# Optimization experiments

Measured on AMD Instinct MI355X. Metric: run time of the kernel, lower is better.

Reference implementation:

```python
import jax, jax.numpy as jnp
import numpy as np

BETA = 0.92
THRESHOLD = 1.0
SLOPE = 25.0  # snntorch surrogate.fast_sigmoid default slope


@jax.custom_vjp
def spike_fn(x):
    # Heaviside forward, fast-sigmoid surrogate backward
    return (x > 0).astype(x.dtype)


def _spike_fwd(x):
    return (x > 0).astype(x.dtype), x


def _spike_bwd(x, g):
    return (g / (SLOPE * jnp.abs(x) + 1.0) ** 2,)


spike_fn.defvjp(_spike_fwd, _spike_bwd)


def _lif(cur, mem_prev):
    # snntorch Leaky (reset_mechanism='subtract'): reset is based on the
    # PREVIOUS membrane and is detached from the graph.
    reset = jax.lax.stop_gradient((mem_prev > THRESHOLD).astype(cur.dtype))
    mem = BETA * mem_prev + cur - reset * THRESHOLD
    spk = spike_fn(mem - THRESHOLD)
    return spk, mem


def setup_inputs() -> dict:
    key = jax.random.key(0)
    ks = jax.random.split(key, 7)
    T, B, D_IN, H = 100, 4096, 9, 96
    return {
        "spike_input": (jax.random.uniform(ks[0], (T, B, D_IN)) < 0.3).astype(jnp.float32),
        "W1": jax.random.normal(ks[1], (H, D_IN), jnp.float32) * (1.0 / np.sqrt(D_IN)),
        "b1": jax.random.normal(ks[2], (H,), jnp.float32) * 0.01,
        "W2": jax.random.normal(ks[3], (H, H), jnp.float32) * (1.0 / np.sqrt(H)),
        "b2": jax.random.normal(ks[4], (H,), jnp.float32) * 0.01,
        "W3": jax.random.normal(ks[5], (H // 2, H), jnp.float32) * (1.0 / np.sqrt(H)),
        "b3": jax.random.normal(ks[6], (H // 2,), jnp.float32) * 0.01,
    }


def reference(spike_input, W1, b1, W2, b2, W3, b3):
    # spike_input: [T, B, input_dim]
    B = spike_input.shape[1]
    H = W1.shape[0]
    H3 = W3.shape[0]
    dt = spike_input.dtype
    init = (jnp.zeros((B, H), dt), jnp.zeros((B, H), dt), jnp.zeros((B, H3), dt))

    def step(carry, x_t):
        m1, m2, m3 = carry
        s1, m1 = _lif(x_t @ W1.T + b1, m1)
        s2, m2 = _lif(s1 @ W2.T + b2, m2)
        s3, m3 = _lif(s2 @ W3.T + b3, m3)
        return (m1, m2, m3), (s3, m3)

    _, (spk_rec, mem_rec) = jax.lax.scan(step, init, spike_input)
    # [T, B, hidden//2] each (fc_out is never applied in the original forward)
    return spk_rec, mem_rec
```

## Files before the change

kernel.cpp:

```cpp
#include <hip/hip_runtime.h>


constexpr int T_STEPS = 100;
constexpr int BATCH   = 4096;
constexpr int D_INP   = 9;
constexpr int H       = 96;
constexpr int H3      = 48;
constexpr int WAVES   = 8;
constexpr int BPW     = 2;
constexpr int NB      = WAVES * BPW;
constexpr int BLOCK   = WAVES * 64;
constexpr int NBLK    = BATCH / NB;

__device__ __forceinline__ float lif_step(float sum, float bias, float& m) {
    const float cur   = __fadd_rn(sum, bias);
    const float mp    = m;
    const float reset = (mp > 1.0f) ? 1.0f : 0.0f;
    const float mn    = __fsub_rn(__fadd_rn(__fmul_rn(0.92f, mp), cur), reset);
    m = mn;
    return mn;
}

#if defined(__has_builtin)
#if __has_builtin(__builtin_amdgcn_mov_dpp)
#define SNN_HAS_DPP 1
#endif
#endif

template <int CTRL>
__device__ __forceinline__ float xadd(float c) {
#ifdef SNN_HAS_DPP
    const int o = __builtin_amdgcn_mov_dpp(__float_as_int(c), CTRL, 0xF, 0xF, false);
    return __fadd_rn(c, __int_as_float(o));
#else
    return __fadd_rn(c, __shfl_xor(c, (CTRL == 0xB1) ? 1 : 2, 64));
#endif
}

__device__ __forceinline__ float quad_red(float c) {
    return xadd<0x4E>(xadd<0xB1>(c));
}

#define UNPACK2(dw, row)                                                      \
    sf[row][0]     = (float)( (dw)        & 255u);                            \
    sf[row][1]     = (float)(((dw) >> 8)  & 255u);                            \
    sf[(row)+1][0] = (float)(((dw) >> 16) & 255u);                            \
    sf[(row)+1][1] = (float)( (dw) >> 24);

#define FMA8(accv, wv, base)                                                  \
    accv[0] = fmaf(wv.x, sf[(base)+0][0], accv[0]);                           \
    accv[1] = fmaf(wv.x, sf[(base)+0][1], accv[1]);                           \
    accv[0] = fmaf(wv.y, sf[(base)+1][0], accv[0]);                           \
    accv[1] = fmaf(wv.y, sf[(base)+1][1], accv[1]);                           \
    accv[0] = fmaf(wv.z, sf[(base)+2][0], accv[0]);                           \
    accv[1] = fmaf(wv.z, sf[(base)+2][1], accv[1]);                           \
    accv[0] = fmaf(wv.w, sf[(base)+3][0], accv[0]);                           \
    accv[1] = fmaf(wv.w, sf[(base)+3][1], accv[1]);

__global__ __launch_bounds__(BLOCK, 2)
void snn_w8(const float* __restrict__ x,
            const float* __restrict__ W1g, const float* __restrict__ b1g,
            const float* __restrict__ W2g, const float* __restrict__ b2g,
            const float* __restrict__ W3g, const float* __restrict__ b3g,
            float* __restrict__ out)
{
    __shared__ __align__(16) float          W2L[36 * 64 * 4];
    __shared__ __align__(16) float          W3L[18 * 64 * 4];
    __shared__ __align__(16) float          W1L[96 * 12];
    __shared__ __align__(16) float          b1L[96], b2L[96], b3L[48];
    __shared__ __align__(16) unsigned short s1u[WAVES][4][24];
    __shared__ __align__(16) unsigned short s2u[WAVES][4][24];

    const int tid = threadIdx.x;
    const int w   = tid >> 6;
    const int l   = tid & 63;
    const int q   = l >> 2;
    const int r   = l & 3;
    const int r01 = r & 1;
    const int bL  = l >> 5;
    const int bg0 = blockIdx.x * NB + w * BPW;

    for (int idx = tid; idx < 36 * 64; idx += BLOCK) {
        const int c = idx >> 6, ll = idx & 63;
        const int s = c / 6, jq = c % 6, qq = ll >> 2, rr = ll & 3;
        #pragma unroll
        for (int jj = 0; jj < 4; ++jj)
            W2L[idx * 4 + jj] = W2g[(16 * s + qq) * H + 16 * jq + 4 * jj + rr];
    }
    for (int idx = tid; idx < 18 * 64; idx += BLOCK) {
        const int c = idx >> 6, ll = idx & 63;
        const int s = c / 6, jq = c % 6, qq = ll >> 2, rr = ll & 3;
        #pragma unroll
        for (int jj = 0; jj < 4; ++jj)
            W3L[idx * 4 + jj] = W3g[(16 * s + qq) * H + 16 * jq + 4 * jj + rr];
    }
    for (int idx = tid; idx < 96 * 12; idx += BLOCK) {
        const int n = idx / 12, k = idx % 12;
        W1L[idx] = (k < 9) ? W1g[n * D_INP + k] : 0.0f;
    }
    if (tid < 96) { b1L[tid] = b1g[tid]; b2L[tid] = b2g[tid]; }
    if (tid < 48) { b3L[tid] = b3g[tid]; }

    float m1[3] = {}, m2[6] = {}, m3[3] = {};

    const float* xp = x + (size_t)(bg0 + bL) * D_INP;
    float xr[D_INP];
    #pragma unroll
    for (int k = 0; k < D_INP; ++k) xr[k] = xp[k];

    float* ps = out + (size_t)(bg0 + r01) * H3 + q;
    float* pm = ps + (size_t)T_STEPS * BATCH * H3;

    __syncthreads();

    unsigned char* s1b = (unsigned char*)&s1u[w][0][0];
    unsigned char* s2b = (unsigned char*)&s2u[w][0][0];

    #pragma unroll 1
    for (int t = 0; t < T_STEPS; ++t) {
        #pragma unroll
        for (int i = 0; i < 3; ++i) {
            const int n1 = (l & 31) + 32 * i;
            const float4 wa = *(const float4*)&W1L[n1 * 12];
            const float4 wb = *(const float4*)&W1L[n1 * 12 + 4];
            const float  w8 = W1L[n1 * 12 + 8];
            const float q0 = __fmul_rn(wa.x, xr[0]);
            const float q1 = __fmul_rn(wa.y, xr[1]);
            const float q2 = __fmul_rn(wa.z, xr[2]);
            const float q3 = __fmul_rn(wa.w, xr[3]);
            const float q4 = __fmul_rn(wb.x, xr[4]);
            const float q5 = __fmul_rn(wb.y, xr[5]);
            const float q6 = __fmul_rn(wb.z, xr[6]);
            const float q7 = __fmul_rn(wb.w, xr[7]);
            const float q8 = __fmul_rn(w8,   xr[8]);
            const float r0 = __fadd_rn(__fadd_rn(q8, q0), q4);
            const float r1 = __fadd_rn(q1, q5);
            const float r2 = __fadd_rn(q2, q6);
            const float r3 = __fadd_rn(q3, q7);
            const float s  = __fadd_rn(__fadd_rn(r0, r1), __fadd_rn(r2, r3));
            const float mn = lif_step(s, b1L[n1], m1[i]);
            s1b[((n1 & 3) * 24 + (n1 >> 2)) * 2 + bL] =
                (mn > 1.0f) ? (unsigned char)1 : (unsigned char)0;
        }
        if (t + 1 < T_STEPS) {
            xp += (size_t)BATCH * D_INP;
            #pragma unroll
            for (int k = 0; k < D_INP; ++k) xr[k] = xp[k];
        }
        asm volatile("s_waitcnt lgkmcnt(0)" ::: "memory");

        {
            float acc[6][2] = {};
            #pragma unroll
            for (int jc = 0; jc < 3; ++jc) {
                const uint4 sp = *(const uint4*)&s1u[w][r][8 * jc];
                float sf[8][2];
                UNPACK2(sp.x, 0) UNPACK2(sp.y, 2) UNPACK2(sp.z, 4) UNPACK2(sp.w, 6)
                #pragma unroll
                for (int s = 0; s < 6; ++s) {
                    const float4 w0 = *(const float4*)&W2L[((s * 6 + 2 * jc)     * 64 + l) * 4];
                    const float4 w1 = *(const float4*)&W2L[((s * 6 + 2 * jc + 1) * 64 + l) * 4];
                    FMA8(acc[s], w0, 0)
                    FMA8(acc[s], w1, 4)
                }
            }
            #pragma unroll
            for (int s = 0; s < 6; ++s) {
                const float g0 = quad_red(acc[s][0]);
                const float g1 = quad_red(acc[s][1]);
                const float sv = r01 ? g1 : g0;
                const float mn = lif_step(sv, b2L[16 * s + q], m2[s]);
                if (r < 2) {
                    const int n2 = 16 * s + q;
                    s2b[((n2 & 3) * 24 + (n2 >> 2)) * 2 + r] =
                        (mn > 1.0f) ? (unsigned char)1 : (unsigned char)0;
                }
            }
        }
        asm volatile("s_waitcnt lgkmcnt(0)" ::: "memory");

        {
            float a3[3][2] = {};
            #pragma unroll
            for (int jc = 0; jc < 3; ++jc) {
                const uint4 sp = *(const uint4*)&s2u[w][r][8 * jc];
                float sf[8][2];
                UNPACK2(sp.x, 0) UNPACK2(sp.y, 2) UNPACK2(sp.z, 4) UNPACK2(sp.w, 6)
                #pragma unroll
                for (int s = 0; s < 3; ++s) {
                    const float4 w0 = *(const float4*)&W3L[((s * 6 + 2 * jc)     * 64 + l) * 4];
                    const float4 w1 = *(const float4*)&W3L[((s * 6 + 2 * jc + 1) * 64 + l) * 4];
                    FMA8(a3[s], w0, 0)
                    FMA8(a3[s], w1, 4)
                }
            }
            #pragma unroll
            for (int s = 0; s < 3; ++s) {
                const float g0 = quad_red(a3[s][0]);
                const float g1 = quad_red(a3[s][1]);
                const float sv = r01 ? g1 : g0;
                const float mn = lif_step(sv, b3L[16 * s + q], m3[s]);
                if (r < 2) {
                    ps[16 * s] = (mn > 1.0f) ? 1.0f : 0.0f;
                    pm[16 * s] = mn;
                }
            }
            ps += (size_t)BATCH * H3;
            pm += (size_t)BATCH * H3;
        }
    }
}

extern "C" void kernel_launch(void* const* d_in, const int* in_sizes, int n_in,
                              void* d_out, int out_size, void* d_ws, size_t ws_size,
                              hipStream_t stream)
{
    const float* x  = (const float*)d_in[0];
    const float* W1 = (const float*)d_in[1];
    const float* b1 = (const float*)d_in[2];
    const float* W2 = (const float*)d_in[3];
    const float* b2 = (const float*)d_in[4];
    const float* W3 = (const float*)d_in[5];
    const float* b3 = (const float*)d_in[6];
    float* out = (float*)d_out;

    snn_w8<<<dim3(NBLK), dim3(BLOCK), 0, stream>>>(
        x, W1, b1, W2, b2, W3, b3, out);
}
```

Baseline: 443.4 us.

## Batch four timesteps per iteration to reuse layer weights from LDS

The time loop is restructured into chunks of four steps. Layer-1 spikes for all four steps are computed first. The W2 and W3 LDS fragments are then loaded once per chunk and applied to all four spike vectors, and the LIF recurrences run sequentially afterwards. W1 and the biases move from shared memory into registers. The goal is to cut LDS weight traffic and the number of per-step waits, at the cost of much higher register pressure, with possible spills under the two-blocks-per-CU launch bound.

```diff
diff --git a/kernel.cpp b/kernel.cpp
--- a/kernel.cpp
+++ b/kernel.cpp
@@ -11,6 +11,7 @@
 constexpr int NB      = WAVES * BPW;
 constexpr int BLOCK   = WAVES * 64;
 constexpr int NBLK    = BATCH / NB;
+constexpr int TC      = 4;
 
 __device__ __forceinline__ float lif_step(float sum, float bias, float& m) {
     const float cur   = __fadd_rn(sum, bias);
@@ -57,19 +58,29 @@
     accv[0] = fmaf(wv.w, sf[(base)+3][0], accv[0]);                           \
     accv[1] = fmaf(wv.w, sf[(base)+3][1], accv[1]);
 
+template <int NS>
+__device__ __forceinline__ void sweep_tp(const uint4 spv,
+                                         const float4* __restrict__ wA,
+                                         const float4* __restrict__ wB,
+                                         float (*__restrict__ acc)[2]) {
+    float sf[8][2];
+    UNPACK2(spv.x, 0) UNPACK2(spv.y, 2) UNPACK2(spv.z, 4) UNPACK2(spv.w, 6)
+    #pragma unroll
+    for (int s = 0; s < NS; ++s) { FMA8(acc[s], wA[s], 0) FMA8(acc[s], wB[s], 4) }
+}
+
+#define FENCE_LGKM() asm volatile("s_waitcnt lgkmcnt(0)" ::: "memory")
+
 __global__ __launch_bounds__(BLOCK, 2)
-void snn_w8(const float* __restrict__ x,
-            const float* __restrict__ W1g, const float* __restrict__ b1g,
-            const float* __restrict__ W2g, const float* __restrict__ b2g,
-            const float* __restrict__ W3g, const float* __restrict__ b3g,
-            float* __restrict__ out)
+void snn_tc4(const float* __restrict__ x,
+             const float* __restrict__ W1g, const float* __restrict__ b1g,
+             const float* __restrict__ W2g, const float* __restrict__ b2g,
+             const float* __restrict__ W3g, const float* __restrict__ b3g,
+             float* __restrict__ out)
 {
     __shared__ __align__(16) float          W2L[36 * 64 * 4];
     __shared__ __align__(16) float          W3L[18 * 64 * 4];
-    __shared__ __align__(16) float          W1L[96 * 12];
-    __shared__ __align__(16) float          b1L[96], b2L[96], b3L[48];
-    __shared__ __align__(16) unsigned short s1u[WAVES][4][24];
-    __shared__ __align__(16) unsigned short s2u[WAVES][4][24];
+    __shared__ __align__(16) unsigned short spk[TC][WAVES][4][24];
 
     const int tid = threadIdx.x;
     const int w   = tid >> 6;
@@ -94,82 +105,94 @@
         for (int jj = 0; jj < 4; ++jj)
             W3L[idx * 4 + jj] = W3g[(16 * s + qq) * H + 16 * jq + 4 * jj + rr];
     }
-    for (int idx = tid; idx < 96 * 12; idx += BLOCK) {
-        const int n = idx / 12, k = idx % 12;
-        W1L[idx] = (k < 9) ? W1g[n * D_INP + k] : 0.0f;
-    }
-    if (tid < 96) { b1L[tid] = b1g[tid]; b2L[tid] = b2g[tid]; }
-    if (tid < 48) { b3L[tid] = b3g[tid]; }
-
+
+    float w1r[3][D_INP], bb1[3];
+    #pragma unroll
+    for (int i = 0; i < 3; ++i) {
+        const int n1 = (l & 31) + 32 * i;
+        #pragma unroll
+        for (int k = 0; k < D_INP; ++k) w1r[i][k] = W1g[n1 * D_INP + k];
+        bb1[i] = b1g[n1];
+    }
+    float bb2[6], bb3[3];
+    #pragma unroll
+    for (int s = 0; s < 6; ++s) bb2[s] = b2g[16 * s + q];
+    #pragma unroll
+    for (int s = 0; s < 3; ++s) bb3[s] = b3g[16 * s + q];
     float m1[3] = {}, m2[6] = {}, m3[3] = {};
 
-    const float* xp = x + (size_t)(bg0 + bL) * D_INP;
-    float xr[D_INP];
-    #pragma unroll
-    for (int k = 0; k < D_INP; ++k) xr[k] = xp[k];
-
-    float* ps = out + (size_t)(bg0 + r01) * H3 + q;
-    float* pm = ps + (size_t)T_STEPS * BATCH * H3;
+    float* out_spk = out;
+    float* out_mem = out + (size_t)T_STEPS * BATCH * H3;
 
     __syncthreads();
 
-    unsigned char* s1b = (unsigned char*)&s1u[w][0][0];
-    unsigned char* s2b = (unsigned char*)&s2u[w][0][0];
-
     #pragma unroll 1
-    for (int t = 0; t < T_STEPS; ++t) {
-        #pragma unroll
-        for (int i = 0; i < 3; ++i) {
-            const int n1 = (l & 31) + 32 * i;
-            const float4 wa = *(const float4*)&W1L[n1 * 12];
-            const float4 wb = *(const float4*)&W1L[n1 * 12 + 4];
-            const float  w8 = W1L[n1 * 12 + 8];
-            const float q0 = __fmul_rn(wa.x, xr[0]);
-            const float q1 = __fmul_rn(wa.y, xr[1]);
-            const float q2 = __fmul_rn(wa.z, xr[2]);
-            const float q3 = __fmul_rn(wa.w, xr[3]);
-            const float q4 = __fmul_rn(wb.x, xr[4]);
-            const float q5 = __fmul_rn(wb.y, xr[5]);
-            const float q6 = __fmul_rn(wb.z, xr[6]);
-            const float q7 = __fmul_rn(wb.w, xr[7]);
-            const float q8 = __fmul_rn(w8,   xr[8]);
-            const float r0 = __fadd_rn(__fadd_rn(q8, q0), q4);
-            const float r1 = __fadd_rn(q1, q5);
-            const float r2 = __fadd_rn(q2, q6);
-            const float r3 = __fadd_rn(q3, q7);
-            const float s  = __fadd_rn(__fadd_rn(r0, r1), __fadd_rn(r2, r3));
-            const float mn = lif_step(s, b1L[n1], m1[i]);
-            s1b[((n1 & 3) * 24 + (n1 >> 2)) * 2 + bL] =
-                (mn > 1.0f) ? (unsigned char)1 : (unsigned char)0;
-        }
-        if (t + 1 < T_STEPS) {
-            xp += (size_t)BATCH * D_INP;
-            #pragma unroll
-            for (int k = 0; k < D_INP; ++k) xr[k] = xp[k];
-        }
-        asm volatile("s_waitcnt lgkmcnt(0)" ::: "memory");
-
-        {
-            float acc[6][2] = {};
-            #pragma unroll
-            for (int jc = 0; jc < 3; ++jc) {
-                const uint4 sp = *(const uint4*)&s1u[w][r][8 * jc];
-                float sf[8][2];
-                UNPACK2(sp.x, 0) UNPACK2(sp.y, 2) UNPACK2(sp.z, 4) UNPACK2(sp.w, 6)
-                #pragma unroll
-                for (int s = 0; s < 6; ++s) {
-                    const float4 w0 = *(const float4*)&W2L[((s * 6 + 2 * jc)     * 64 + l) * 4];
-                    const float4 w1 = *(const float4*)&W2L[((s * 6 + 2 * jc + 1) * 64 + l) * 4];
-                    FMA8(acc[s], w0, 0)
-                    FMA8(acc[s], w1, 4)
-                }
-            }
+    for (int tc = 0; tc < T_STEPS; tc += TC) {
+        float xr[TC][D_INP];
+        const float* xp = x + ((size_t)tc * BATCH + bg0 + bL) * D_INP;
+        #pragma unroll
+        for (int tp = 0; tp < TC; ++tp) {
+            #pragma unroll
+            for (int k = 0; k < D_INP; ++k)
+                xr[tp][k] = xp[(size_t)tp * BATCH * D_INP + k];
+        }
+
+        #pragma unroll
+        for (int tp = 0; tp < TC; ++tp) {
+            unsigned char* s1b = (unsigned char*)&spk[tp][w][0][0];
+            #pragma unroll
+            for (int i = 0; i < 3; ++i) {
+                const int n1 = (l & 31) + 32 * i;
+                const float q0 = __fmul_rn(w1r[i][0], xr[tp][0]);
+                const float q1 = __fmul_rn(w1r[i][1], xr[tp][1]);
+                const float q2 = __fmul_rn(w1r[i][2], xr[tp][2]);
+                const float q3 = __fmul_rn(w1r[i][3], xr[tp][3]);
+                const float q4 = __fmul_rn(w1r[i][4], xr[tp][4]);
+                const float q5 = __fmul_rn(w1r[i][5], xr[tp][5]);
+                const float q6 = __fmul_rn(w1r[i][6], xr[tp][6]);
+                const float q7 = __fmul_rn(w1r[i][7], xr[tp][7]);
+                const float q8 = __fmul_rn(w1r[i][8], xr[tp][8]);
+                const float r0 = __fadd_rn(__fadd_rn(q8, q0), q4);
+                const float r1 = __fadd_rn(q1, q5);
+                const float r2 = __fadd_rn(q2, q6);
+                const float r3 = __fadd_rn(q3, q7);
+                const float s  = __fadd_rn(__fadd_rn(r0, r1), __fadd_rn(r2, r3));
+                const float mn = lif_step(s, bb1[i], m1[i]);
+                s1b[((n1 & 3) * 24 + (n1 >> 2)) * 2 + bL] =
+                    (mn > 1.0f) ? (unsigned char)1 : (unsigned char)0;
+            }
+        }
+        FENCE_LGKM();
+
+        float acc[TC][6][2] = {};
+        #pragma unroll
+        for (int jc = 0; jc < 3; ++jc) {
+            const uint4 sp0 = *(const uint4*)&spk[0][w][r][8 * jc];
+            const uint4 sp1 = *(const uint4*)&spk[1][w][r][8 * jc];
+            const uint4 sp2 = *(const uint4*)&spk[2][w][r][8 * jc];
+            const uint4 sp3 = *(const uint4*)&spk[3][w][r][8 * jc];
+            float4 wA[6], wB[6];
             #pragma unroll
             for (int s = 0; s < 6; ++s) {
-                const float g0 = quad_red(acc[s][0]);
-                const float g1 = quad_red(acc[s][1]);
+                wA[s] = *(const float4*)&W2L[((s * 6 + 2 * jc)     * 64 + l) * 4];
+                wB[s] = *(const float4*)&W2L[((s * 6 + 2 * jc + 1) * 64 + l) * 4];
+            }
+            sweep_tp<6>(sp0, wA, wB, acc[0]);
+            sweep_tp<6>(sp1, wA, wB, acc[1]);
+            sweep_tp<6>(sp2, wA, wB, acc[2]);
+            sweep_tp<6>(sp3, wA, wB, acc[3]);
+        }
+        FENCE_LGKM();
+
+        #pragma unroll
+        for (int tp = 0; tp < TC; ++tp) {
+            unsigned char* s2b = (unsigned char*)&spk[tp][w][0][0];
+            #pragma unroll
+            for (int s = 0; s < 6; ++s) {
+                const float g0 = quad_red(acc[tp][s][0]);
+                const float g1 = quad_red(acc[tp][s][1]);
                 const float sv = r01 ? g1 : g0;
-                const float mn = lif_step(sv, b2L[16 * s + q], m2[s]);
+                const float mn = lif_step(sv, bb2[s], m2[s]);
                 if (r < 2) {
                     const int n2 = 16 * s + q;
                     s2b[((n2 & 3) * 24 + (n2 >> 2)) * 2 + r] =
@@ -177,37 +200,44 @@
                 }
             }
         }
-        asm volatile("s_waitcnt lgkmcnt(0)" ::: "memory");
-
-        {
-            float a3[3][2] = {};
-            #pragma unroll
-            for (int jc = 0; jc < 3; ++jc) {
-                const uint4 sp = *(const uint4*)&s2u[w][r][8 * jc];
-                float sf[8][2];
-                UNPACK2(sp.x, 0) UNPACK2(sp.y, 2) UNPACK2(sp.z, 4) UNPACK2(sp.w, 6)
-                #pragma unroll
-                for (int s = 0; s < 3; ++s) {
-                    const float4 w0 = *(const float4*)&W3L[((s * 6 + 2 * jc)     * 64 + l) * 4];
-                    const float4 w1 = *(const float4*)&W3L[((s * 6 + 2 * jc + 1) * 64 + l) * 4];
-                    FMA8(a3[s], w0, 0)
-                    FMA8(a3[s], w1, 4)
+        FENCE_LGKM();
+
+        float a3[TC][3][2] = {};
+        #pragma unroll
+        for (int jc = 0; jc < 3; ++jc) {
+            const uint4 sp0 = *(const uint4*)&spk[0][w][r][8 * jc];
+            const uint4 sp1 = *(const uint4*)&spk[1][w][r][8 * jc];
+            const uint4 sp2 = *(const uint4*)&spk[2][w][r][8 * jc];
+            const uint4 sp3 = *(const uint4*)&spk[3][w][r][8 * jc];
+            float4 wA[3], wB[3];
+            #pragma unroll
+            for (int s = 0; s < 3; ++s) {
+                wA[s] = *(const float4*)&W3L[((s * 6 + 2 * jc)     * 64 + l) * 4];
+                wB[s] = *(const float4*)&W3L[((s * 6 + 2 * jc + 1) * 64 + l) * 4];
+            }
+            sweep_tp<3>(sp0, wA, wB, a3[0]);
+            sweep_tp<3>(sp1, wA, wB, a3[1]);
+            sweep_tp<3>(sp2, wA, wB, a3[2]);
+            sweep_tp<3>(sp3, wA, wB, a3[3]);
+        }
+
+        #pragma unroll
+        for (int tp = 0; tp < TC; ++tp) {
+            #pragma unroll
+            for (int s = 0; s < 3; ++s) {
+                const float g0 = quad_red(a3[tp][s][0]);
+                const float g1 = quad_red(a3[tp][s][1]);
+                const float sv = r01 ? g1 : g0;
+                const float mn = lif_step(sv, bb3[s], m3[s]);
+                if (r < 2) {
+                    const size_t ob =
+                        ((size_t)(tc + tp) * BATCH + bg0 + r) * H3 + 16 * s + q;
+                    out_spk[ob] = (mn > 1.0f) ? 1.0f : 0.0f;
+                    out_mem[ob] = mn;
                 }
             }
-            #pragma unroll
-            for (int s = 0; s < 3; ++s) {
-                const float g0 = quad_red(a3[s][0]);
-                const float g1 = quad_red(a3[s][1]);
-                const float sv = r01 ? g1 : g0;
-                const float mn = lif_step(sv, b3L[16 * s + q], m3[s]);
-                if (r < 2) {
-                    ps[16 * s] = (mn > 1.0f) ? 1.0f : 0.0f;
-                    pm[16 * s] = mn;
-                }
-            }
-            ps += (size_t)BATCH * H3;
-            pm += (size_t)BATCH * H3;
-        }
+        }
+        FENCE_LGKM();
     }
 }
 
@@ -224,6 +254,6 @@
     const float* b3 = (const float*)d_in[6];
     float* out = (float*)d_out;
 
-    snn_w8<<<dim3(NBLK), dim3(BLOCK), 0, stream>>>(
+    snn_tc4<<<dim3(NBLK), dim3(BLOCK), 0, stream>>>(
         x, W1, b1, W2, b2, W3, b3, out);
 }
```

Result: slower. 558.3 us (+25.9%).
